# Kernel optimization log

Measured on AMD Instinct MI355X. Metric: run time of the kernel, lower is better.

The kernel has to match this reference:

```python
import jax, jax.numpy as jnp
import numpy as np

N, E, F_IN, H, D = 50000, 800000, 128, 4, 32


def setup_inputs() -> dict:
    key = jax.random.key(0)
    k_x, k_e, k_w, k_al, k_ar = jax.random.split(key, 5)
    x = jax.random.normal(k_x, (N, F_IN), dtype=jnp.float32)
    edge_index = jax.random.randint(k_e, (2, E), 0, N, dtype=jnp.int32).astype(jnp.int64)
    # xavier-uniform-like scales
    s_w = float(np.sqrt(6.0 / (F_IN + H * D)))
    s_a = float(np.sqrt(6.0 / (D + 1)))
    W = jax.random.uniform(k_w, (F_IN, H * D), jnp.float32, -s_w, s_w)
    att_l = jax.random.uniform(k_al, (H, D), jnp.float32, -s_a, s_a)
    att_r = jax.random.uniform(k_ar, (H, D), jnp.float32, -s_a, s_a)
    bias = jnp.zeros((H * D,), jnp.float32)
    return {"x": x, "edge_index": edge_index, "W": W, "att_l": att_l, "att_r": att_r, "bias": bias}


def reference(x, edge_index, W, att_l, att_r, bias):
    num_nodes = x.shape[0]
    n_heads, head_dim = att_l.shape
    h = (x @ W).reshape(num_nodes, n_heads, head_dim)          # [N,H,D]
    alpha_l = jnp.einsum('nhd,hd->nh', h, att_l)               # [N,H]
    alpha_r = jnp.einsum('nhd,hd->nh', h, att_r)               # [N,H]
    from_idx, to_idx = edge_index[0], edge_index[1]
    att = alpha_l[from_idx] + alpha_r[to_idx]                  # [E,H]
    att = jax.nn.leaky_relu(att, negative_slope=0.2)
    # segment softmax over edges grouped by destination node (shift by global
    # per-head max, exactly as the source's _softmax effectively does)
    att = att - jax.lax.stop_gradient(jnp.max(att, axis=0, keepdims=True))
    ex = jnp.exp(att)                                          # [E,H]
    denom = jax.ops.segment_sum(ex, to_idx, num_segments=num_nodes)  # [N,H]
    att_n = ex / (denom[to_idx] + 1e-9)                        # [E,H]
    # scatter-weighted aggregation: out[n] = sum_{e: to=n} att[e] * h[from[e]]
    msgs = att_n[:, :, None] * h[from_idx]                     # [E,H,D]
    out = jax.ops.segment_sum(msgs, to_idx, num_segments=num_nodes)  # [N,H,D]
    out = out.reshape(num_nodes, n_heads * head_dim) + bias
    return out
```

## Files before the change

kernel.cpp:

```cpp
#include <hip/hip_runtime.h>
#include <cstdint>

#define N_NODES 50000
#define N_EDGES 800000
#define F_IN    128
#define N_HEADS 4
#define HEAD_DIM 32
#define F_OUT   128

#define NBUCK   391
#define NPB     128
#define KA_GRID 256
#define EPB     (N_EDGES / KA_GRID)
#define CAPA    32
#define REC_CAP 2560
#define STAGE_CAP REC_CAP
#define NGEMM   1563

typedef unsigned int uint32;
typedef unsigned short ushort;
typedef __attribute__((ext_vector_type(8))) short short8v;
typedef __attribute__((ext_vector_type(4))) float float4v;

__device__ __forceinline__ ushort f2bf(float f) {
    uint32 u = __float_as_uint(f);
    return (ushort)((u + 0x7FFFu + ((u >> 16) & 1u)) >> 16);
}

__device__ __forceinline__ int block_scan_excl_256(int v, int* p_total)
{
    const int t = threadIdx.x, lane = t & 63, wv = t >> 6;
    int incl = v;
#pragma unroll
    for (int d = 1; d < 64; d <<= 1) {
        int u = __shfl_up(incl, d);
        if (lane >= d) incl += u;
    }
    __shared__ int wsum[4];
    if (lane == 63) wsum[wv] = incl;
    __syncthreads();
    int woff = 0;
#pragma unroll
    for (int j = 0; j < 4; ++j) {
        int s = wsum[j];
        if (j < wv) woff += s;
    }
    if (p_total) *p_total = wsum[0] + wsum[1] + wsum[2] + wsum[3];
    __syncthreads();
    return woff + incl - v;
}

__global__ __launch_bounds__(256) void k_prep(const float* __restrict__ W,
    ushort* __restrict__ WT_hi, ushort* __restrict__ WT_lo)
{
    const int id = blockIdx.x * 256 + threadIdx.x;
    if (id < F_IN * F_OUT) {
        const int n = id & 127, k = id >> 7;
        const float w = W[k * F_OUT + n];
        const ushort hi = f2bf(w);
        const float hif = __uint_as_float((uint32)hi << 16);
        WT_hi[n * F_IN + k] = hi;
        WT_lo[n * F_IN + k] = f2bf(w - hif);
    }
}

__global__ __launch_bounds__(256, 4) void k_bin_gemm(
    const int* __restrict__ ei, const float* __restrict__ x,
    const ushort* __restrict__ WT_hi, const ushort* __restrict__ WT_lo,
    const float* __restrict__ attl, const float* __restrict__ attr,
    uint2* __restrict__ priv, int* __restrict__ cnts,
    uint32* __restrict__ hbq, float* __restrict__ aLp, float* __restrict__ aRp)
{
    if (blockIdx.x < KA_GRID) {
        __shared__ int cur[NBUCK];
        const int sb = blockIdx.x, t = threadIdx.x;
        for (int bb = t; bb < NBUCK; bb += 256) cur[bb] = 0;
        __syncthreads();
        const int e0 = sb * EPB;
        for (int i = t; i < EPB; i += 256) {
            const int from = ei[e0 + i];
            const int to   = ei[N_EDGES + e0 + i];
            const int b = to >> 7;
            const int slot = atomicAdd(&cur[b], 1);
            if (slot < CAPA)
                priv[((size_t)b * KA_GRID + sb) * CAPA + slot] =
                    make_uint2((uint32)from, (uint32)to);
        }
        __syncthreads();
        for (int bb = t; bb < NBUCK; bb += 256)
            cnts[sb * NBUCK + bb] = min(cur[bb], CAPA);
        return;
    }

    const int bid   = blockIdx.x - KA_GRID;
    const int lane  = threadIdx.x & 63;
    const int wv    = threadIdx.x >> 6;
    const int strip = bid * 2 + (wv >> 1);
    const int half  = wv & 1;
    const int q     = lane >> 4;
    const int c15   = lane & 15;
    const int row0  = strip * 16;
    if (row0 >= N_NODES) return;

    const float* xrow = x + (size_t)(row0 + c15) * F_IN + q * 8;
    short8v ahi[4], alo[4];
#pragma unroll
    for (int kt = 0; kt < 4; ++kt) {
        const float4 f0 = *(const float4*)(xrow + kt * 32);
        const float4 f1 = *(const float4*)(xrow + kt * 32 + 4);
        const float fs[8] = {f0.x, f0.y, f0.z, f0.w, f1.x, f1.y, f1.z, f1.w};
#pragma unroll
        for (int j = 0; j < 8; ++j) {
            const ushort hi = f2bf(fs[j]);
            const float hif = __uint_as_float((uint32)hi << 16);
            ahi[kt][j] = (short)hi;
            alo[kt][j] = (short)f2bf(fs[j] - hif);
        }
    }

    const int nt0 = half * 4;
    short8v bh_c[4], bl_c[4];
    {
        const ushort* bhb = WT_hi + ((nt0 * 16 + c15) << 7) + q * 8;
        const ushort* blb = WT_lo + ((nt0 * 16 + c15) << 7) + q * 8;
#pragma unroll
        for (int kt = 0; kt < 4; ++kt) {
            bh_c[kt] = *(const short8v*)(bhb + kt * 32);
            bl_c[kt] = *(const short8v*)(blb + kt * 32);
        }
    }

    float4v acc[4];
#pragma unroll
    for (int j = 0; j < 4; ++j) {
        short8v bh_n[4], bl_n[4];
        if (j < 3) {
            const ushort* bhb = WT_hi + (((nt0 + j + 1) * 16 + c15) << 7) + q * 8;
            const ushort* blb = WT_lo + (((nt0 + j + 1) * 16 + c15) << 7) + q * 8;
#pragma unroll
            for (int kt = 0; kt < 4; ++kt) {
                bh_n[kt] = *(const short8v*)(bhb + kt * 32);
                bl_n[kt] = *(const short8v*)(blb + kt * 32);
            }
        }
        float4v a = {0.f, 0.f, 0.f, 0.f};
#pragma unroll
        for (int kt = 0; kt < 4; ++kt) {
            a = __builtin_amdgcn_mfma_f32_16x16x32_bf16(ahi[kt], bh_c[kt], a, 0, 0, 0);
            a = __builtin_amdgcn_mfma_f32_16x16x32_bf16(alo[kt], bh_c[kt], a, 0, 0, 0);
            a = __builtin_amdgcn_mfma_f32_16x16x32_bf16(ahi[kt], bl_c[kt], a, 0, 0, 0);
        }
        acc[j] = a;
        if (j < 3) {
#pragma unroll
            for (int kt = 0; kt < 4; ++kt) { bh_c[kt] = bh_n[kt]; bl_c[kt] = bl_n[kt]; }
        }
    }

#pragma unroll
    for (int j = 0; j < 2; ++j) {
#pragma unroll
        for (int r = 0; r < 4; ++r) {
            const uint32 d = (uint32)f2bf(acc[j][r]) | ((uint32)f2bf(acc[j + 2][r]) << 16);
            hbq[(size_t)(row0 + q * 4 + r) * 64 + half * 32 + j * 16 + c15] = d;
        }
    }

    float aLacc[4][2] = {{0.f}}, aRacc[4][2] = {{0.f}};
#pragma unroll
    for (int j = 0; j < 4; ++j) {
        const int col = (nt0 + j) * 16 + c15;
        const float alv = attl[col];
        const float arv = attr[col];
        const int hl = j >> 1;
#pragma unroll
        for (int r = 0; r < 4; ++r) {
            aLacc[r][hl] = fmaf(acc[j][r], alv, aLacc[r][hl]);
            aRacc[r][hl] = fmaf(acc[j][r], arv, aRacc[r][hl]);
        }
    }
#pragma unroll
    for (int r = 0; r < 4; ++r) {
#pragma unroll
        for (int hl = 0; hl < 2; ++hl) {
            float vl = aLacc[r][hl], vr = aRacc[r][hl];
#pragma unroll
            for (int d = 1; d < 16; d <<= 1) {
                vl += __shfl_xor(vl, d);
                vr += __shfl_xor(vr, d);
            }
            if (c15 == hl) {
                const int row = row0 + q * 4 + r;
                aLp[row * N_HEADS + half * 2 + hl] = vl;
                aRp[row * N_HEADS + half * 2 + hl] = vr;
            }
        }
    }
}

__global__ __launch_bounds__(256) void k_build(const uint2* __restrict__ priv,
    const int* __restrict__ cnts,
    int* __restrict__ count, int* __restrict__ offsets, int* __restrict__ rec_from)
{
    __shared__ uint2 stage[STAGE_CAP];
    __shared__ int so_s[256], cts_s[256];
    __shared__ int hist[NPB], curn[NPB];
    const int b = blockIdx.x, t = threadIdx.x;

    const int ct = cnts[t * NBUCK + b];
    int total;
    const int so = block_scan_excl_256(ct, &total);
    so_s[t] = ct ? so : 0;
    so_s[t] = so;
    cts_s[t] = ct;
    if (t < NPB) hist[t] = 0;
    __syncthreads();

    const uint2* pbase = priv + (size_t)b * KA_GRID * CAPA;
    for (int idx = t; idx < KA_GRID * CAPA; idx += 256) {
        const int sb = idx >> 5;
        const int sl = idx & 31;
        if (sl < cts_s[sb]) {
            const int p = so_s[sb] + sl;
            if (p < STAGE_CAP) stage[p] = pbase[idx];
        }
    }
    __syncthreads();

    const int S = min(total, STAGE_CAP);
    for (int i = t; i < S; i += 256) atomicAdd(&hist[stage[i].y & (NPB - 1)], 1);
    __syncthreads();

    const int hv = (t < NPB) ? hist[t] : 0;
    int tot2;
    const int lo = block_scan_excl_256(hv, &tot2);
    const int rbase = b * REC_CAP;
    const int n = b * NPB + t;
    if (t < NPB && n < N_NODES) {
        count[n]   = hv;
        offsets[n] = rbase + lo;
    }
    if (t < NPB) curn[t] = lo;
    __syncthreads();

    for (int i = t; i < S; i += 256) {
        const uint2 e = stage[i];
        const int pos = atomicAdd(&curn[e.y & (NPB - 1)], 1);
        rec_from[rbase + pos] = (int)e.x;
    }
}

__global__ __launch_bounds__(256) void k_agg(const int* __restrict__ rec_from,
    const int* __restrict__ count, const int* __restrict__ offsets,
    const float* __restrict__ aLp, const float* __restrict__ aRp,
    const uint32* __restrict__ hbq,
    const float* __restrict__ bias, float* __restrict__ out)
{
    const int lane = threadIdx.x & 63;
    const int n = blockIdx.x * 4 + (threadIdx.x >> 6);
    if (n >= N_NODES) return;
    const int cnt  = count[n];
    const int off  = offsets[n];
    const int hsel = (lane >> 5) * 2;
    const int l31  = lane & 31;
    const int gsel = lane & 32;
    const float2 arv = *(const float2*)&aRp[n * N_HEADS + hsel];
    float ax = 0.f, ay = 0.f, ds0 = 0.f, ds1 = 0.f;

    for (int base = 0; base < cnt; base += 32) {
        const int m = min(32, cnt - base);
        int vf = 0;
        float e0p = 0.f, e1p = 0.f;
        if (l31 < m) {
            vf = rec_from[off + base + l31];
            const float2 af = *(const float2*)&aLp[vf * N_HEADS + hsel];
            float t0 = af.x + arv.x; t0 = (t0 > 0.f) ? t0 : 0.2f * t0;
            float t1 = af.y + arv.y; t1 = (t1 > 0.f) ? t1 : 0.2f * t1;
            e0p = __expf(t0);
            e1p = __expf(t1);
        }
        int i = 0;
        for (; i + 8 <= m; i += 8) {
            int f[8]; uint32 h[8]; float e0[8], e1[8];
#pragma unroll
            for (int j = 0; j < 8; ++j) {
                const int s = gsel | (i + j);
                f[j]  = __shfl(vf, s);
                e0[j] = __shfl(e0p, s);
                e1[j] = __shfl(e1p, s);
            }
#pragma unroll
            for (int j = 0; j < 8; ++j) h[j] = hbq[(size_t)f[j] * 64 + lane];
#pragma unroll
            for (int j = 0; j < 8; ++j) {
                ax = fmaf(e0[j], __uint_as_float(h[j] << 16), ax);
                ay = fmaf(e1[j], __uint_as_float(h[j] & 0xFFFF0000u), ay);
                ds0 += e0[j]; ds1 += e1[j];
            }
        }
        for (; i + 4 <= m; i += 4) {
            int f[4]; uint32 h[4]; float e0[4], e1[4];
#pragma unroll
            for (int j = 0; j < 4; ++j) {
                const int s = gsel | (i + j);
                f[j]  = __shfl(vf, s);
                e0[j] = __shfl(e0p, s);
                e1[j] = __shfl(e1p, s);
            }
#pragma unroll
            for (int j = 0; j < 4; ++j) h[j] = hbq[(size_t)f[j] * 64 + lane];
#pragma unroll
            for (int j = 0; j < 4; ++j) {
                ax = fmaf(e0[j], __uint_as_float(h[j] << 16), ax);
                ay = fmaf(e1[j], __uint_as_float(h[j] & 0xFFFF0000u), ay);
                ds0 += e0[j]; ds1 += e1[j];
            }
        }
        for (; i < m; ++i) {
            const int s = gsel | i;
            const int f = __shfl(vf, s);
            const uint32 hv = hbq[(size_t)f * 64 + lane];
            const float e0 = __shfl(e0p, s), e1 = __shfl(e1p, s);
            ax = fmaf(e0, __uint_as_float(hv << 16), ax);
            ay = fmaf(e1, __uint_as_float(hv & 0xFFFF0000u), ay);
            ds0 += e0; ds1 += e1;
        }
    }
    const float inv0 = 1.0f / (ds0 + 1e-9f);
    const float inv1 = 1.0f / (ds1 + 1e-9f);
    const int d0 = (lane < 32) ? lane : lane + 32;
    out[n * F_OUT + d0]      = ax * inv0 + bias[d0];
    out[n * F_OUT + d0 + 32] = ay * inv1 + bias[d0 + 32];
}

extern "C" void kernel_launch(void* const* d_in, const int* in_sizes, int n_in,
                              void* d_out, int out_size, void* d_ws, size_t ws_size,
                              hipStream_t stream)
{
    const float* x    = (const float*)d_in[0];
    const int*   ei   = (const int*)d_in[1];
    const float* W    = (const float*)d_in[2];
    const float* attl = (const float*)d_in[3];
    const float* attr = (const float*)d_in[4];
    const float* bias = (const float*)d_in[5];
    float* out = (float*)d_out;

    char* p = (char*)d_ws;
    auto carve = [&](size_t bytes) -> char* {
        char* q = p;
        p += (bytes + 255) & ~size_t(255);
        return q;
    };
    uint32* hbq      = (uint32*)carve((size_t)N_NODES * 64 * 4);
    uint2*  priv     = (uint2*)carve((size_t)NBUCK * KA_GRID * CAPA * 8);
    int*    rec_from = (int*)carve((size_t)NBUCK * REC_CAP * 4);
    ushort* WT_hi    = (ushort*)carve((size_t)F_IN * F_OUT * 2);
    ushort* WT_lo    = (ushort*)carve((size_t)F_IN * F_OUT * 2);
    float*  aLp      = (float*)carve((size_t)N_NODES * N_HEADS * 4);
    float*  aRp      = (float*)carve((size_t)N_NODES * N_HEADS * 4);
    int*    cnts     = (int*)carve((size_t)KA_GRID * NBUCK * 4);
    int*    count    = (int*)carve((size_t)N_NODES * 4);
    int*    offsets  = (int*)carve((size_t)N_NODES * 4);

    k_prep<<<64, 256, 0, stream>>>(W, WT_hi, WT_lo);
    k_bin_gemm<<<KA_GRID + NGEMM, 256, 0, stream>>>(ei, x, WT_hi, WT_lo,
                                                    attl, attr, priv, cnts,
                                                    hbq, aLp, aRp);
    k_build<<<NBUCK, 256, 0, stream>>>(priv, cnts, count, offsets, rec_from);
    k_agg<<<(N_NODES + 3) / 4, 256, 0, stream>>>(rec_from, count, offsets,
                                                 aLp, aRp, hbq, bias, out);
}
```

Before: 172.9 us.

## Give each wave a full 16-row strip and stage x via LDS

The GEMM part now assigns one wave per 16-row strip computing all 128 output columns, where before two waves split the columns. This removes the duplicated x loads and bf16 hi/lo splitting of the A operand. x rows are brought into shared memory with global_load_lds so the per-lane fragments come from LDS rather than strided global reads. The packed hbq layout, the alpha positions and the output column mapping are changed to match. The cost is more accumulator registers (eight tiles per wave), the loss of W prefetch double-buffering, and a 32 KB LDS allocation that now also applies to the binning blocks and may lower occupancy.

```diff
diff --git a/kernel.cpp b/kernel.cpp
--- a/kernel.cpp
+++ b/kernel.cpp
@@ -15,17 +15,22 @@
 #define CAPA    32
 #define REC_CAP 2560
 #define STAGE_CAP REC_CAP
-#define NGEMM   1563
+#define NSTRIP  (N_NODES / 16)
+#define NGEMM   ((NSTRIP + 3) / 4)
 
 typedef unsigned int uint32;
 typedef unsigned short ushort;
 typedef __attribute__((ext_vector_type(8))) short short8v;
 typedef __attribute__((ext_vector_type(4))) float float4v;
 
+typedef __attribute__((address_space(1))) const float gfloat;
+typedef __attribute__((address_space(3))) float lfloat;
+
 __device__ __forceinline__ ushort f2bf(float f) {
     uint32 u = __float_as_uint(f);
     return (ushort)((u + 0x7FFFu + ((u >> 16) & 1u)) >> 16);
 }
+
 
 __device__ __forceinline__ int block_scan_excl_256(int v, int* p_total)
 {
@@ -71,8 +76,10 @@
     uint2* __restrict__ priv, int* __restrict__ cnts,
     uint32* __restrict__ hbq, float* __restrict__ aLp, float* __restrict__ aRp)
 {
+    __shared__ float xl[4][16 * 128];
+    __shared__ int cur[NBUCK];
+
     if (blockIdx.x < KA_GRID) {
-        __shared__ int cur[NBUCK];
         const int sb = blockIdx.x, t = threadIdx.x;
         for (int bb = t; bb < NBUCK; bb += 256) cur[bb] = 0;
         __syncthreads();
@@ -95,19 +102,28 @@
     const int bid   = blockIdx.x - KA_GRID;
     const int lane  = threadIdx.x & 63;
     const int wv    = threadIdx.x >> 6;
-    const int strip = bid * 2 + (wv >> 1);
-    const int half  = wv & 1;
+    const int strip = bid * 4 + wv;
+    if (strip >= NSTRIP) return;
     const int q     = lane >> 4;
     const int c15   = lane & 15;
     const int row0  = strip * 16;
-    if (row0 >= N_NODES) return;
-
-    const float* xrow = x + (size_t)(row0 + c15) * F_IN + q * 8;
+
+    const float* gbase = x + (size_t)row0 * F_IN;
+    float* lbase = &xl[wv][0];
+#pragma unroll
+    for (int i = 0; i < 8; ++i) {
+        __builtin_amdgcn_global_load_lds(
+            (gfloat*)(gbase + i * 256 + lane * 4),
+            (lfloat*)(lbase + i * 256), 16, 0, 0);
+    }
+    __asm volatile("s_waitcnt vmcnt(0)" ::: "memory");
+
+    const float* arow = lbase + c15 * F_IN + q * 8;
     short8v ahi[4], alo[4];
 #pragma unroll
     for (int kt = 0; kt < 4; ++kt) {
-        const float4 f0 = *(const float4*)(xrow + kt * 32);
-        const float4 f1 = *(const float4*)(xrow + kt * 32 + 4);
+        const float4 f0 = *(const float4*)(arow + kt * 32);
+        const float4 f1 = *(const float4*)(arow + kt * 32 + 4);
         const float fs[8] = {f0.x, f0.y, f0.z, f0.w, f1.x, f1.y, f1.z, f1.w};
 #pragma unroll
         for (int j = 0; j < 8; ++j) {
@@ -118,81 +134,59 @@
         }
     }
 
-    const int nt0 = half * 4;
-    short8v bh_c[4], bl_c[4];
-    {
-        const ushort* bhb = WT_hi + ((nt0 * 16 + c15) << 7) + q * 8;
-        const ushort* blb = WT_lo + ((nt0 * 16 + c15) << 7) + q * 8;
+    float4v acc[8];
+#pragma unroll
+    for (int nt = 0; nt < 8; ++nt) {
+        float4v a = {0.f, 0.f, 0.f, 0.f};
+        const ushort* bhb = WT_hi + ((nt * 16 + c15) << 7) + q * 8;
+        const ushort* blb = WT_lo + ((nt * 16 + c15) << 7) + q * 8;
 #pragma unroll
         for (int kt = 0; kt < 4; ++kt) {
-            bh_c[kt] = *(const short8v*)(bhb + kt * 32);
-            bl_c[kt] = *(const short8v*)(blb + kt * 32);
-        }
-    }
-
-    float4v acc[4];
-#pragma unroll
-    for (int j = 0; j < 4; ++j) {
-        short8v bh_n[4], bl_n[4];
-        if (j < 3) {
-            const ushort* bhb = WT_hi + (((nt0 + j + 1) * 16 + c15) << 7) + q * 8;
-            const ushort* blb = WT_lo + (((nt0 + j + 1) * 16 + c15) << 7) + q * 8;
-#pragma unroll
-            for (int kt = 0; kt < 4; ++kt) {
-                bh_n[kt] = *(const short8v*)(bhb + kt * 32);
-                bl_n[kt] = *(const short8v*)(blb + kt * 32);
-            }
-        }
-        float4v a = {0.f, 0.f, 0.f, 0.f};
-#pragma unroll
-        for (int kt = 0; kt < 4; ++kt) {
-            a = __builtin_amdgcn_mfma_f32_16x16x32_bf16(ahi[kt], bh_c[kt], a, 0, 0, 0);
-            a = __builtin_amdgcn_mfma_f32_16x16x32_bf16(alo[kt], bh_c[kt], a, 0, 0, 0);
-            a = __builtin_amdgcn_mfma_f32_16x16x32_bf16(ahi[kt], bl_c[kt], a, 0, 0, 0);
-        }
-        acc[j] = a;
-        if (j < 3) {
-#pragma unroll
-            for (int kt = 0; kt < 4; ++kt) { bh_c[kt] = bh_n[kt]; bl_c[kt] = bl_n[kt]; }
-        }
-    }
-
-#pragma unroll
-    for (int j = 0; j < 2; ++j) {
+            const short8v bh = *(const short8v*)(bhb + kt * 32);
+            const short8v bl = *(const short8v*)(blb + kt * 32);
+            a = __builtin_amdgcn_mfma_f32_16x16x32_bf16(ahi[kt], bh, a, 0, 0, 0);
+            a = __builtin_amdgcn_mfma_f32_16x16x32_bf16(alo[kt], bh, a, 0, 0, 0);
+            a = __builtin_amdgcn_mfma_f32_16x16x32_bf16(ahi[kt], bl, a, 0, 0, 0);
+        }
+        acc[nt] = a;
+    }
+
+#pragma unroll
+    for (int nt = 0; nt < 4; ++nt) {
 #pragma unroll
         for (int r = 0; r < 4; ++r) {
-            const uint32 d = (uint32)f2bf(acc[j][r]) | ((uint32)f2bf(acc[j + 2][r]) << 16);
-            hbq[(size_t)(row0 + q * 4 + r) * 64 + half * 32 + j * 16 + c15] = d;
-        }
-    }
-
-    float aLacc[4][2] = {{0.f}}, aRacc[4][2] = {{0.f}};
-#pragma unroll
-    for (int j = 0; j < 4; ++j) {
-        const int col = (nt0 + j) * 16 + c15;
-        const float alv = attl[col];
-        const float arv = attr[col];
-        const int hl = j >> 1;
+            const uint32 d = (uint32)f2bf(acc[nt][r]) | ((uint32)f2bf(acc[nt + 4][r]) << 16);
+            hbq[(size_t)(row0 + q * 4 + r) * 64 + nt * 16 + c15] = d;
+        }
+    }
+
+    float aLacc[4][4] = {{0.f}}, aRacc[4][4] = {{0.f}};
+#pragma unroll
+    for (int nt = 0; nt < 8; ++nt) {
+        const float alv = attl[nt * 16 + c15];
+        const float arv = attr[nt * 16 + c15];
+        const int hh = nt >> 1;
 #pragma unroll
         for (int r = 0; r < 4; ++r) {
-            aLacc[r][hl] = fmaf(acc[j][r], alv, aLacc[r][hl]);
-            aRacc[r][hl] = fmaf(acc[j][r], arv, aRacc[r][hl]);
+            aLacc[r][hh] = fmaf(acc[nt][r], alv, aLacc[r][hh]);
+            aRacc[r][hh] = fmaf(acc[nt][r], arv, aRacc[r][hh]);
         }
     }
 #pragma unroll
     for (int r = 0; r < 4; ++r) {
 #pragma unroll
-        for (int hl = 0; hl < 2; ++hl) {
-            float vl = aLacc[r][hl], vr = aRacc[r][hl];
+        for (int hh = 0; hh < 4; ++hh) {
+            float vl = aLacc[r][hh], vr = aRacc[r][hh];
 #pragma unroll
             for (int d = 1; d < 16; d <<= 1) {
                 vl += __shfl_xor(vl, d);
                 vr += __shfl_xor(vr, d);
             }
-            if (c15 == hl) {
+            if (c15 == hh) {
                 const int row = row0 + q * 4 + r;
-                aLp[row * N_HEADS + half * 2 + hl] = vl;
-                aRp[row * N_HEADS + half * 2 + hl] = vr;
+                const int pos = (hh & 1) * 2 + (hh >> 1);
+                aLp[row * N_HEADS + pos] = vl;
+                aRp[row * N_HEADS + pos] = vr;
             }
         }
     }
@@ -210,7 +204,6 @@
     const int ct = cnts[t * NBUCK + b];
     int total;
     const int so = block_scan_excl_256(ct, &total);
-    so_s[t] = ct ? so : 0;
     so_s[t] = so;
     cts_s[t] = ct;
     if (t < NPB) hist[t] = 0;
@@ -328,9 +321,8 @@
     }
     const float inv0 = 1.0f / (ds0 + 1e-9f);
     const float inv1 = 1.0f / (ds1 + 1e-9f);
-    const int d0 = (lane < 32) ? lane : lane + 32;
-    out[n * F_OUT + d0]      = ax * inv0 + bias[d0];
-    out[n * F_OUT + d0 + 32] = ay * inv1 + bias[d0 + 32];
+    out[n * F_OUT + lane]      = ax * inv0 + bias[lane];
+    out[n * F_OUT + 64 + lane] = ay * inv1 + bias[64 + lane];
 }
 
 extern "C" void kernel_launch(void* const* d_in, const int* in_sizes, int n_in,
```

Measured after the change: 174.0 us. No clear change (+0.6%).
